# Kernel optimization log

Measured on AMD Instinct MI355X. Metric: run time of the kernel, lower is better.

Reference implementation:

```python
import jax, jax.numpy as jnp
import numpy as np

NHEAD = 16
DHEAD = 128  # dim_embed // nhead
ROPE_BASE = 10000.0


def rmsnorm(x, g):
    eps = jnp.finfo(x.dtype).eps  # torch nn.RMSNorm default eps=None -> dtype eps
    return x * jax.lax.rsqrt(jnp.mean(x * x, axis=-1, keepdims=True) + eps) * g


def rope(x):
    # torchtune-style interleaved RoPE. x: [B,S,H,D]
    B, S, H, D = x.shape
    freqs = 1.0 / (ROPE_BASE ** (jnp.arange(0, D, 2, dtype=jnp.float32) / D))  # [D/2]
    ang = jnp.arange(S, dtype=jnp.float32)[:, None] * freqs[None, :]           # [S,D/2]
    cos = jnp.cos(ang)[None, :, None, :]
    sin = jnp.sin(ang)[None, :, None, :]
    x1, x2 = x[..., 0::2], x[..., 1::2]
    return jnp.stack([x1 * cos - x2 * sin, x1 * sin + x2 * cos], axis=-1).reshape(B, S, H, D)


def setup_inputs() -> dict:
    key = jax.random.key(0)
    B, S, E, C = 4, 2048, 2048, 512
    ks = jax.random.split(key, 9)
    std = 0.02
    h = jax.random.normal(ks[0], (B, S, E), jnp.float32)
    w_d_kv = jax.random.normal(ks[1], (C, E), jnp.float32) * std
    w_u_k = jax.random.normal(ks[2], (E, C), jnp.float32) * std
    w_u_v = jax.random.normal(ks[3], (E, C), jnp.float32) * std
    w_d_q = jax.random.normal(ks[4], (C, E), jnp.float32) * std
    w_u_q = jax.random.normal(ks[5], (E, C), jnp.float32) * std
    w_kr = jax.random.normal(ks[6], (E, E), jnp.float32) * std
    w_qr = jax.random.normal(ks[7], (E, C), jnp.float32) * std
    w_o = jax.random.normal(ks[8], (E, E), jnp.float32) * std
    g1 = jnp.ones((C,), jnp.float32)
    g2 = jnp.ones((C,), jnp.float32)
    g3 = jnp.ones((E,), jnp.float32)
    return {"h": h, "w_d_kv": w_d_kv, "w_u_k": w_u_k, "w_u_v": w_u_v,
            "w_d_q": w_d_q, "w_u_q": w_u_q, "w_kr": w_kr, "w_qr": w_qr,
            "w_o": w_o, "g1": g1, "g2": g2, "g3": g3}


def reference(h, w_d_kv, w_u_k, w_u_v, w_d_q, w_u_q, w_kr, w_qr, w_o, g1, g2, g3):
    # Eval (inference) path of MLA with absorbed weights; no kv/kr cache.
    B, S, E = h.shape
    cq = rmsnorm(h @ w_d_q.T, g1)          # [B,S,C]
    ckv = rmsnorm(h @ w_d_kv.T, g2)        # [B,S,C]
    qr = rope((cq @ w_qr.T).reshape(B, S, NHEAD, DHEAD)).reshape(B, S, E)
    kr = rope((h @ w_kr.T).reshape(B, S, NHEAD, DHEAD)).reshape(B, S, E)
    # absorbed_w_q = (w_d_q.T @ w_u_q.T) @ w_u_k : [E,C]
    absorbed_w_q = (w_d_q.T @ w_u_q.T) @ w_u_k
    # absorbed_w_o = w_u_v.T @ w_o.T : [C,E]
    absorbed_w_o = w_u_v.T @ w_o.T
    aq = h @ absorbed_w_q                  # [B,S,C]  (note: raw h, as in source)
    scores = jnp.einsum('bsc,btc->bst', aq, ckv) + jnp.einsum('bse,bte->bst', qr, kr)
    attn = jax.nn.softmax(scores / np.float32(np.sqrt(NHEAD + DHEAD)), axis=-1)
    o = jnp.einsum('bst,btc->bsc', attn, ckv)
    u = rmsnorm(o @ absorbed_w_o, g3)      # [B,S,E]
    return (u, ckv, kr)
```

## Files before the change

kernel.cpp:

```cpp
#include <hip/hip_runtime.h>
#include <stdint.h>

typedef __attribute__((ext_vector_type(8))) short bf16x8;
typedef __attribute__((ext_vector_type(8))) unsigned short u16x8;
typedef __attribute__((ext_vector_type(4))) float floatx4;

__device__ __forceinline__ uint16_t f2bf(float f) {
  union { float f; uint32_t u; } v; v.f = f;
  uint32_t r = v.u + 0x7fffu + ((v.u >> 16) & 1u);
  return (uint16_t)(r >> 16);
}
__device__ __forceinline__ float bf2f(uint16_t b) {
  union { uint32_t u; float f; } v; v.u = ((uint32_t)b) << 16;
  return v.f;
}
__device__ __forceinline__ float ld_as_float(float v) { return v; }
__device__ __forceinline__ float ld_as_float(uint16_t v) { return bf2f(v); }

__device__ __forceinline__ void mfma16(floatx4& d, bf16x8 a, bf16x8 b) {
  asm("v_mfma_f32_16x16x32_bf16 %0, %1, %2, %0" : "+v"(d) : "v"(a), "v"(b));
}

#define FENCE() asm volatile("" ::: "memory")
#define SCHED() __builtin_amdgcn_sched_barrier(0)
#define SBAR()                                  \
  do {                                          \
    FENCE();                                    \
    __builtin_amdgcn_sched_barrier(0);          \
    __builtin_amdgcn_s_barrier();               \
    __builtin_amdgcn_sched_barrier(0);          \
    FENCE();                                    \
  } while (0)

template<int MODE>
__global__ void __launch_bounds__(512, 1) gemm256v3(
    const uint16_t* __restrict__ A, const uint16_t* __restrict__ B,
    void* __restrict__ C0v, void* __restrict__ C1v, void* __restrict__ C2v,
    int K, int lda, int ldb, int ldc,
    long sA, long sB, long sC, int swzG)
{
  __shared__ __attribute__((aligned(16))) char lds[131072];
  const int tid = threadIdx.x;
  const int w = tid >> 6, l = tid & 63;
  const int wm = w >> 2, wn = w & 3;

  const int gx = gridDim.x;
  const int nwg = gx * gridDim.y;
  int id = blockIdx.y * gx + blockIdx.x;
  if ((nwg & 7) == 0) id = (id & 7) * (nwg >> 3) + (id >> 3);
  const int grp = gx * swzG;
  const int ing = id % grp;
  const long bm = (long)(ing / swzG) * 256;
  const long bn = ((long)(id / grp) * swzG + (ing % swzG)) * 256;
  A += (long)blockIdx.z * sA;
  B += (long)blockIdx.z * sB;

  const int scol = (((l & 3) ^ ((l >> 3) & 3)) << 3);
  const uint16_t* gA = A + (bm + w * 16 + (l >> 2)) * (long)lda + scol;
  const uint16_t* gB = B + (bn + w * 16 + (l >> 2)) * (long)ldb + scol;
  const int ldsw = w * 1024;

#define STG_A3(slot, k0, r)                                                    \
  __builtin_amdgcn_global_load_lds(gA + (k0) + (long)(r) * 128 * lda,          \
      (uint16_t*)(lds + (slot) * 32768 + (r) * 8192 + ldsw), 16, 0, 0)
#define STG_B3(slot, k0, r)                                                    \
  __builtin_amdgcn_global_load_lds(gB + (k0) + (long)(r) * 128 * ldb,          \
      (uint16_t*)(lds + (slot) * 32768 + 16384 + (r) * 8192 + ldsw), 16, 0, 0)

  const int lr = l & 15;
  const int chunkx = (((l >> 4) ^ ((lr >> 1) & 3)) << 4);
  const int aoff = (wm * 128 + lr) * 64 + chunkx;
  const int boff = 16384 + (wn * 64 + lr) * 64 + chunkx;

  floatx4 acc[8][4];
#pragma unroll
  for (int i = 0; i < 8; i++)
#pragma unroll
    for (int j = 0; j < 4; j++) acc[i][j] = (floatx4){0.f, 0.f, 0.f, 0.f};

  const int nt = K >> 5;
#pragma unroll
  for (int tt = 0; tt < 3; tt++) {
    STG_A3(tt, tt * 32, 0); STG_A3(tt, tt * 32, 1);
    STG_B3(tt, tt * 32, 0); STG_B3(tt, tt * 32, 1);
  }
  asm volatile("s_waitcnt vmcnt(8)" ::: "memory");
  SBAR();

  bf16x8 Bf[4], Bfn[4], Af0[4], Af1[4];
#pragma unroll
  for (int j = 0; j < 4; j++) Bf[j] = *(const bf16x8*)(lds + boff + j * 1024);
#pragma unroll
  for (int i = 0; i < 4; i++) Af0[i] = *(const bf16x8*)(lds + aoff + i * 1024);

  for (int t = 0; t < nt; t++) {
    const char* Ls = lds + (t & 3) * 32768;
    const char* Ln = lds + ((t + 1) & 3) * 32768;
    const long pk0 = (long)(t + 3) << 5;
    const int pslot = (t + 3) & 3;
    const bool pf = (t + 3 < nt);

#pragma unroll
    for (int i = 0; i < 4; i++) Af1[i] = *(const bf16x8*)(Ls + aoff + (4 + i) * 1024);
    SCHED();
    if (pf) { STG_A3(pslot, pk0, 0); STG_A3(pslot, pk0, 1); }
    asm volatile("s_waitcnt lgkmcnt(4)" ::: "memory");
    SCHED();
    __builtin_amdgcn_s_setprio(1);
#pragma unroll
    for (int i = 0; i < 4; i++)
#pragma unroll
      for (int j = 0; j < 4; j++) mfma16(acc[i][j], Af0[i], Bf[j]);
    __builtin_amdgcn_s_setprio(0);
    SCHED();

    if (t + 3 < nt)      asm volatile("s_waitcnt vmcnt(6)" ::: "memory");
    else if (t + 2 < nt) asm volatile("s_waitcnt vmcnt(4)" ::: "memory");
    else if (t + 1 < nt) asm volatile("s_waitcnt vmcnt(0)" ::: "memory");
    asm volatile("s_waitcnt lgkmcnt(0)" ::: "memory");
    SBAR();

    if (t + 1 < nt) {
#pragma unroll
      for (int j = 0; j < 4; j++) Bfn[j] = *(const bf16x8*)(Ln + boff + j * 1024);
#pragma unroll
      for (int i = 0; i < 4; i++) Af0[i] = *(const bf16x8*)(Ln + aoff + i * 1024);
    }
    SCHED();
    if (pf) { STG_B3(pslot, pk0, 0); STG_B3(pslot, pk0, 1); }
    SCHED();
    __builtin_amdgcn_s_setprio(1);
#pragma unroll
    for (int i = 0; i < 4; i++)
#pragma unroll
      for (int j = 0; j < 4; j++) mfma16(acc[4 + i][j], Af1[i], Bf[j]);
    __builtin_amdgcn_s_setprio(0);
    SCHED();
#pragma unroll
    for (int j = 0; j < 4; j++) Bf[j] = Bfn[j];
  }
#undef STG_A3
#undef STG_B3

  const long crow = bm + wm * 128 + ((l >> 4) * 4);
  const long ccol = bn + wn * 64 + (l & 15);
  if constexpr (MODE == 0) {
    float* C = (float*)C0v + (long)blockIdx.z * sC;
#pragma unroll
    for (int i = 0; i < 8; i++)
#pragma unroll
      for (int r = 0; r < 4; r++) {
        long row = crow + i * 16 + r;
#pragma unroll
        for (int j = 0; j < 4; j++) C[row * (long)ldc + ccol + j * 16] = acc[i][j][r];
      }
  } else if constexpr (MODE == 1) {
    uint16_t* C = (uint16_t*)C0v + (long)blockIdx.z * sC;
#pragma unroll
    for (int i = 0; i < 8; i++)
#pragma unroll
      for (int r = 0; r < 4; r++) {
        long row = crow + i * 16 + r;
#pragma unroll
        for (int j = 0; j < 4; j++) C[row * (long)ldc + ccol + j * 16] = f2bf(acc[i][j][r]);
      }
  } else if constexpr (MODE == 3) {
    const float s = 1.0f / 12.0f;
    uint16_t* C = (uint16_t*)C0v + (long)blockIdx.z * sC;
#pragma unroll
    for (int i = 0; i < 8; i++)
#pragma unroll
      for (int r = 0; r < 4; r++) {
        long row = crow + i * 16 + r;
#pragma unroll
        for (int j = 0; j < 4; j++) C[row * (long)ldc + ccol + j * 16] = f2bf(acc[i][j][r] * s);
      }
  } else {
    if (bn < 512) {
      uint16_t* C = (uint16_t*)C0v;
#pragma unroll
      for (int i = 0; i < 8; i++)
#pragma unroll
        for (int r = 0; r < 4; r++) {
          long row = crow + i * 16 + r;
#pragma unroll
          for (int j = 0; j < 4; j++) C[row * 512 + ccol + j * 16] = f2bf(acc[i][j][r]);
        }
    } else if (bn < 1024) {
      float* C = (float*)C1v;
      const long cc = ccol - 512;
#pragma unroll
      for (int i = 0; i < 8; i++)
#pragma unroll
        for (int r = 0; r < 4; r++) {
          long row = crow + i * 16 + r;
#pragma unroll
          for (int j = 0; j < 4; j++) C[row * 512 + cc + j * 16] = acc[i][j][r];
        }
    } else {
      uint16_t* C = (uint16_t*)C2v;
      const long cc = ccol - 1024;
#pragma unroll
      for (int i = 0; i < 8; i++)
#pragma unroll
        for (int r = 0; r < 4; r++) {
          long row = crow + i * 16 + r;
#pragma unroll
          for (int j = 0; j < 4; j++) C[row * 2560 + cc + j * 16] = f2bf(acc[i][j][r]);
        }
    }
  }
}

template<int OUTB>
__global__ void __launch_bounds__(512, 2) gemm256(
    const uint16_t* __restrict__ A, const uint16_t* __restrict__ B,
    void* __restrict__ Cv, int K, int lda, int ldb, int ldc,
    long sA, long sB, long sC)
{
  __shared__ __attribute__((aligned(16))) char lds[147456];
  const int tid = threadIdx.x;
  const int w = tid >> 6, l = tid & 63;
  const int wm = w >> 1, wn = w & 1;

  const int gx = gridDim.x;
  const int nwg = gx * gridDim.y;
  int id = blockIdx.y * gx + blockIdx.x;
  if ((nwg & 7) == 0) id = (id & 7) * (nwg >> 3) + (id >> 3);
  const long bm = (long)(id % gx) * 256;
  const long bn = (long)(id / gx) * 128;
  A += (long)blockIdx.z * sA;
  B += (long)blockIdx.z * sB;

  const int sr = l >> 3;
  const int sc = l & 7;
  const int scol = ((sc ^ sr) << 3);
  const uint16_t* gA = A + (bm + w * 8 + sr) * (long)lda + scol;
  const uint16_t* gB = B + (bn + w * 8 + sr) * (long)ldb + scol;
  const int ldsw = w * 1024;

#define STAGE_A(bufi, k0, r)                                                     \
  __builtin_amdgcn_global_load_lds(gA + (k0) + (long)(r) * 64 * lda,             \
      (uint16_t*)(lds + (bufi) * 49152 + (r) * 8192 + ldsw), 16, 0, 0)
#define STAGE_B(bufi, k0, r)                                                     \
  __builtin_amdgcn_global_load_lds(gB + (k0) + (long)(r) * 64 * ldb,             \
      (uint16_t*)(lds + (bufi) * 49152 + 32768 + (r) * 8192 + ldsw), 16, 0, 0)

  const int lr = l & 15;
  const int kk = (l >> 4) << 4;
  const int msk = (l & 7) << 4;
  const int ko0 = kk ^ msk;
  const int ko1 = (64 + kk) ^ msk;
  const int arow = (wm * 64 + lr) * 128;
  const int brow = (wn * 64 + lr) * 128;

  floatx4 acc[4][4];
#pragma unroll
  for (int i = 0; i < 4; i++)
#pragma unroll
    for (int j = 0; j < 4; j++) acc[i][j] = (floatx4){0.f, 0.f, 0.f, 0.f};

  const int nt = K >> 6;
#pragma unroll
  for (int r = 0; r < 4; r++) STAGE_A(0, 0, r);
#pragma unroll
  for (int r = 0; r < 2; r++) STAGE_B(0, 0, r);
#pragma unroll
  for (int r = 0; r < 4; r++) STAGE_A(1, 64, r);
#pragma unroll
  for (int r = 0; r < 2; r++) STAGE_B(1, 64, r);
  asm volatile("s_waitcnt vmcnt(6)" ::: "memory");
  SBAR();

  bf16x8 af0[4], bf0[4], af1[4], bf1[4];
  {
    const char* LA = lds + arow;
    const char* LB = lds + 32768 + brow;
#pragma unroll
    for (int i = 0; i < 4; i++) af0[i] = *(const bf16x8*)(LA + i * 2048 + ko0);
#pragma unroll
    for (int j = 0; j < 4; j++) bf0[j] = *(const bf16x8*)(LB + j * 2048 + ko0);
  }

  for (int t = 0; t < nt; t++) {
    const int buf = t % 3;
    const int pbuf = (t + 2) % 3;
    const long pk0 = (long)(t + 2) << 6;
    const char* LA = lds + buf * 49152 + arow;
    const char* LB = lds + buf * 49152 + 32768 + brow;
    const bool pf = (t + 2 < nt);

    if (pf) { STAGE_A(pbuf, pk0, 0); STAGE_A(pbuf, pk0, 1); STAGE_B(pbuf, pk0, 0); }
#pragma unroll
    for (int i = 0; i < 4; i++) af1[i] = *(const bf16x8*)(LA + i * 2048 + ko1);
#pragma unroll
    for (int j = 0; j < 4; j++) bf1[j] = *(const bf16x8*)(LB + j * 2048 + ko1);
    SCHED();
    __builtin_amdgcn_s_setprio(1);
#pragma unroll
    for (int i = 0; i < 4; i++)
#pragma unroll
      for (int j = 0; j < 4; j++) mfma16(acc[i][j], af0[i], bf0[j]);
    __builtin_amdgcn_s_setprio(0);
    SCHED();

    if (pf) { STAGE_A(pbuf, pk0, 2); STAGE_A(pbuf, pk0, 3); STAGE_B(pbuf, pk0, 1); }
    if (t < nt - 2) asm volatile("s_waitcnt vmcnt(6) lgkmcnt(0)" ::: "memory");
    else            asm volatile("s_waitcnt vmcnt(0) lgkmcnt(0)" ::: "memory");
    SBAR();
    if (t < nt - 1) {
      const char* LAn = lds + ((t + 1) % 3) * 49152 + arow;
      const char* LBn = lds + ((t + 1) % 3) * 49152 + 32768 + brow;
#pragma unroll
      for (int i = 0; i < 4; i++) af0[i] = *(const bf16x8*)(LAn + i * 2048 + ko0);
#pragma unroll
      for (int j = 0; j < 4; j++) bf0[j] = *(const bf16x8*)(LBn + j * 2048 + ko0);
    }
    SCHED();
    __builtin_amdgcn_s_setprio(1);
#pragma unroll
    for (int i = 0; i < 4; i++)
#pragma unroll
      for (int j = 0; j < 4; j++) mfma16(acc[i][j], af1[i], bf1[j]);
    __builtin_amdgcn_s_setprio(0);
    SCHED();
  }
#undef STAGE_A
#undef STAGE_B

  const long crow = bm + wm * 64 + ((l >> 4) * 4);
  const long ccol = bn + wn * 64 + (l & 15);
  if constexpr (OUTB == 0) {
    float* C = (float*)Cv + (long)blockIdx.z * sC;
#pragma unroll
    for (int i = 0; i < 4; i++)
#pragma unroll
      for (int r = 0; r < 4; r++) {
        long row = crow + i * 16 + r;
#pragma unroll
        for (int j = 0; j < 4; j++) C[row * (long)ldc + ccol + j * 16] = acc[i][j][r];
      }
  } else {
    uint16_t* C = (uint16_t*)Cv + (long)blockIdx.z * sC;
#pragma unroll
    for (int i = 0; i < 4; i++)
#pragma unroll
      for (int r = 0; r < 4; r++) {
        long row = crow + i * 16 + r;
#pragma unroll
        for (int j = 0; j < 4; j++) C[row * (long)ldc + ccol + j * 16] = f2bf(acc[i][j][r]);
      }
  }
}

template<int OUTB>
__global__ void __launch_bounds__(256) gemm_bt(
    const uint16_t* __restrict__ A, const uint16_t* __restrict__ B,
    void* __restrict__ Cv, int K, int lda, int ldb, int ldc,
    long sA, long sB, long sC)
{
  __shared__ alignas(16) uint16_t As[4096];
  __shared__ alignas(16) uint16_t Bs[4096];
  const int tid = threadIdx.x;
  const int w = tid >> 6, l = tid & 63;
  const int wr = w >> 1, wc = w & 1;
  const long bm = (long)blockIdx.x * 128, bn = (long)blockIdx.y * 128;
  A += (long)blockIdx.z * sA;
  B += (long)blockIdx.z * sB;

  const uint16_t* ga0 = A + (bm + w * 16 + (l >> 2)) * (long)lda + (l & 3) * 8;
  const uint16_t* ga1 = ga0 + 64L * lda;
  const uint16_t* gb0 = B + (bn + w * 16 + (l >> 2)) * (long)ldb + (l & 3) * 8;
  const uint16_t* gb1 = gb0 + 64L * ldb;
  uint16_t* la0 = &As[w * 512];
  uint16_t* la1 = &As[2048 + w * 512];
  uint16_t* lb0 = &Bs[w * 512];
  uint16_t* lb1 = &Bs[2048 + w * 512];

  floatx4 acc[4][4];
#pragma unroll
  for (int i = 0; i < 4; i++)
#pragma unroll
    for (int j = 0; j < 4; j++) acc[i][j] = (floatx4){0.f, 0.f, 0.f, 0.f};

  const int rA = (wr * 64 + (l & 15)) * 32 + (l >> 4) * 8;
  const int rB = (wc * 64 + (l & 15)) * 32 + (l >> 4) * 8;

  for (int k0 = 0; k0 < K; k0 += 32) {
    __builtin_amdgcn_global_load_lds(ga0, la0, 16, 0, 0);
    __builtin_amdgcn_global_load_lds(ga1, la1, 16, 0, 0);
    __builtin_amdgcn_global_load_lds(gb0, lb0, 16, 0, 0);
    __builtin_amdgcn_global_load_lds(gb1, lb1, 16, 0, 0);
    ga0 += 32; ga1 += 32; gb0 += 32; gb1 += 32;
    __syncthreads();
    bf16x8 af[4], bfr[4];
#pragma unroll
    for (int i = 0; i < 4; i++) af[i] = *(const bf16x8*)&As[rA + i * 512];
#pragma unroll
    for (int j = 0; j < 4; j++) bfr[j] = *(const bf16x8*)&Bs[rB + j * 512];
#pragma unroll
    for (int i = 0; i < 4; i++)
#pragma unroll
      for (int j = 0; j < 4; j++) mfma16(acc[i][j], af[i], bfr[j]);
    __syncthreads();
  }

  const long crow = bm + wr * 64 + ((l >> 4) * 4);
  const long ccol = bn + wc * 64 + (l & 15);
  if constexpr (OUTB == 0) {
    float* C = (float*)Cv + (long)blockIdx.z * sC;
#pragma unroll
    for (int i = 0; i < 4; i++)
#pragma unroll
      for (int r = 0; r < 4; r++) {
        long row = crow + i * 16 + r;
#pragma unroll
        for (int j = 0; j < 4; j++) C[row * (long)ldc + ccol + j * 16] = acc[i][j][r];
      }
  } else {
    uint16_t* C = (uint16_t*)Cv + (long)blockIdx.z * sC;
#pragma unroll
    for (int i = 0; i < 4; i++)
#pragma unroll
      for (int r = 0; r < 4; r++) {
        long row = crow + i * 16 + r;
#pragma unroll
        for (int j = 0; j < 4; j++) C[row * (long)ldc + ccol + j * 16] = f2bf(acc[i][j][r]);
      }
  }
}

__global__ void __launch_bounds__(256) reduceK(const float* __restrict__ in,
                                               uint16_t* __restrict__ out,
                                               long n, int S, long stride) {
  long i = ((long)blockIdx.x * 256 + threadIdx.x) * 4;
  if (i >= n) return;
  float4 s = *(const float4*)(in + i);
  for (int k = 1; k < S; k++) {
    float4 t = *(const float4*)(in + k * stride + i);
    s.x += t.x; s.y += t.y; s.z += t.z; s.w += t.w;
  }
  ushort4 o; o.x = f2bf(s.x); o.y = f2bf(s.y); o.z = f2bf(s.z); o.w = f2bf(s.w);
  *(ushort4*)(out + i) = o;
}

__global__ void __launch_bounds__(256) prep_all(
    const float* __restrict__ h,
    const float* __restrict__ wdq, const float* __restrict__ wdkv,
    const float* __restrict__ wqr, const float* __restrict__ wkr,
    const float* __restrict__ wo,
    uint16_t* __restrict__ hb,
    uint16_t* __restrict__ wdq_b, uint16_t* __restrict__ wdkv_b,
    uint16_t* __restrict__ wqr_b, uint16_t* __restrict__ wkr_b,
    uint16_t* __restrict__ wo_b, float2* __restrict__ rtab)
{
  const int b = blockIdx.x;
  if (b < 27648) {
    const float* src; uint16_t* dst; long off;
    if (b < 16384)      { src = h;    dst = hb;     off = b; }
    else if (b < 17408) { src = wdq;  dst = wdq_b;  off = b - 16384; }
    else if (b < 18432) { src = wdkv; dst = wdkv_b; off = b - 17408; }
    else if (b < 19456) { src = wqr;  dst = wqr_b;  off = b - 18432; }
    else if (b < 23552) { src = wkr;  dst = wkr_b;  off = b - 19456; }
    else                { src = wo;   dst = wo_b;   off = b - 23552; }
    long i = (off * 256 + threadIdx.x) * 4;
    float4 v = *(const float4*)(src + i);
    ushort4 o; o.x = f2bf(v.x); o.y = f2bf(v.y); o.z = f2bf(v.z); o.w = f2bf(v.w);
    *(ushort4*)(dst + i) = o;
  } else {
    int idx = (b - 27648) * 256 + threadIdx.x;
    int s = idx >> 6, fi = idx & 63;
    float f = powf(10000.0f, -(float)fi * (1.0f / 64.0f));
    float ang = (float)s * f;
    rtab[idx] = make_float2(cosf(ang), sinf(ang));
  }
}

template<typename TIN>
__global__ void __launch_bounds__(256) transpose_to_bf16(
    const TIN* __restrict__ in, uint16_t* __restrict__ out,
    int ld_in, int ld_out, long sIn, long sOut)
{
  __shared__ float tile[32][33];
  in += (long)blockIdx.z * sIn;
  out += (long)blockIdx.z * sOut;
  const int rb = blockIdx.y * 32, cb = blockIdx.x * 32;
#pragma unroll
  for (int i = 0; i < 32; i += 8)
    tile[threadIdx.y + i][threadIdx.x] =
        ld_as_float(in[(long)(rb + threadIdx.y + i) * ld_in + cb + threadIdx.x]);
  __syncthreads();
#pragma unroll
  for (int i = 0; i < 32; i += 8)
    out[(long)(cb + threadIdx.y + i) * ld_out + rb + threadIdx.x] =
        f2bf(tile[threadIdx.x][threadIdx.y + i]);
}

template<int PT, typename TIN>
__global__ void __launch_bounds__(256) rmsnorm_k(
    const TIN* __restrict__ in, const float* __restrict__ g,
    float* __restrict__ out_f, uint16_t* __restrict__ out_b, int ld_b)
{
  constexpr int DIM = PT * 256;
  __shared__ float sm[9];
  const TIN* x = in + (long)blockIdx.x * DIM;
  const int base = threadIdx.x * PT;
  float v[PT];
  if constexpr (sizeof(TIN) == 2) {
    if constexpr (PT >= 8) {
#pragma unroll
      for (int i = 0; i < PT; i += 8) {
        u16x8 t = *(const u16x8*)&x[base + i];
#pragma unroll
        for (int q = 0; q < 8; q++) v[i + q] = bf2f(t[q]);
      }
    } else {
#pragma unroll
      for (int i = 0; i < PT; i += 2) {
        ushort2 t = *(const ushort2*)&x[base + i];
        v[i] = bf2f(t.x); v[i + 1] = bf2f(t.y);
      }
    }
  } else if constexpr (PT == 2) {
    float2 t = *(const float2*)&x[base]; v[0] = t.x; v[1] = t.y;
  } else {
#pragma unroll
    for (int i = 0; i < PT; i += 4) {
      float4 t = *(const float4*)&x[base + i];
      v[i] = t.x; v[i + 1] = t.y; v[i + 2] = t.z; v[i + 3] = t.w;
    }
  }
  float ss = 0.f;
#pragma unroll
  for (int i = 0; i < PT; i++) ss += v[i] * v[i];
#pragma unroll
  for (int o = 32; o; o >>= 1) ss += __shfl_down(ss, o);
  if ((threadIdx.x & 63) == 0) sm[threadIdx.x >> 6] = ss;
  __syncthreads();
  if (threadIdx.x == 0)
    sm[8] = rsqrtf((sm[0] + sm[1] + sm[2] + sm[3]) * (1.0f / DIM) + 1.1920929e-7f);
  __syncthreads();
  const float sc = sm[8];
#pragma unroll
  for (int i = 0; i < PT; i++) {
    float y = v[i] * sc * g[base + i];
    if (out_f) out_f[(long)blockIdx.x * DIM + base + i] = y;
    if (out_b) out_b[(long)blockIdx.x * ld_b + base + i] = f2bf(y);
  }
}

template<bool WF32>
__global__ void __launch_bounds__(256) rope_k(
    const uint16_t* __restrict__ in, uint16_t* __restrict__ outb,
    float* __restrict__ outf, const float2* __restrict__ tab)
{
  long idx = (long)blockIdx.x * 256 + threadIdx.x;
  int r = (int)(idx >> 10);
  int pp = (int)idx & 1023;
  int s = r & 2047;
  int fi = pp & 63;
  ushort2 xv = *(const ushort2*)(in + ((long)r << 11) + 2 * pp);
  float x0 = bf2f(xv.x), x1 = bf2f(xv.y);
  float2 cs = tab[(s << 6) + fi];
  float y0 = x0 * cs.x - x1 * cs.y;
  float y1 = x0 * cs.y + x1 * cs.x;
  ushort2 ov; ov.x = f2bf(y0); ov.y = f2bf(y1);
  *(ushort2*)(outb + (long)r * 2560 + 512 + 2 * pp) = ov;
  if (WF32) *(float2*)(outf + ((long)r << 11) + 2 * pp) = make_float2(y0, y1);
}

__global__ void __launch_bounds__(256) softmax_k(const uint16_t* __restrict__ sc,
                                                 uint16_t* __restrict__ attn) {
  __shared__ float sm[9];
  const uint16_t* x = sc + ((long)blockIdx.x << 11);
  const int base = threadIdx.x * 8;
  float v[8];
  u16x8 t = *(const u16x8*)&x[base];
#pragma unroll
  for (int i = 0; i < 8; i++) v[i] = bf2f(t[i]);
  float m = -1e30f;
#pragma unroll
  for (int i = 0; i < 8; i++) m = fmaxf(m, v[i]);
#pragma unroll
  for (int o = 32; o; o >>= 1) m = fmaxf(m, __shfl_down(m, o));
  if ((threadIdx.x & 63) == 0) sm[threadIdx.x >> 6] = m;
  __syncthreads();
  if (threadIdx.x == 0)
    sm[8] = fmaxf(fmaxf(sm[0], sm[1]), fmaxf(sm[2], sm[3]));
  __syncthreads();
  m = sm[8];
  __syncthreads();
  float ss = 0.f;
#pragma unroll
  for (int i = 0; i < 8; i++) { v[i] = __expf(v[i] - m); ss += v[i]; }
#pragma unroll
  for (int o = 32; o; o >>= 1) ss += __shfl_down(ss, o);
  if ((threadIdx.x & 63) == 0) sm[threadIdx.x >> 6] = ss;
  __syncthreads();
  if (threadIdx.x == 0) sm[8] = 1.0f / (sm[0] + sm[1] + sm[2] + sm[3]);
  __syncthreads();
  const float r = sm[8];
  ushort4 o1, o2;
  o1.x = f2bf(v[0] * r); o1.y = f2bf(v[1] * r); o1.z = f2bf(v[2] * r); o1.w = f2bf(v[3] * r);
  o2.x = f2bf(v[4] * r); o2.y = f2bf(v[5] * r); o2.z = f2bf(v[6] * r); o2.w = f2bf(v[7] * r);
  uint16_t* dst = attn + ((long)blockIdx.x << 11) + base;
  *(ushort4*)dst = o1;
  *(ushort4*)(dst + 4) = o2;
}

extern "C" void kernel_launch(void* const* d_in, const int* in_sizes, int n_in,
                              void* d_out, int out_size, void* d_ws, size_t ws_size,
                              hipStream_t stream) {
  (void)in_sizes; (void)n_in; (void)out_size; (void)ws_size;
  const float* h    = (const float*)d_in[0];
  const float* wdkv = (const float*)d_in[1];
  const float* wuk  = (const float*)d_in[2];
  const float* wuv  = (const float*)d_in[3];
  const float* wdq  = (const float*)d_in[4];
  const float* wuq  = (const float*)d_in[5];
  const float* wkr  = (const float*)d_in[6];
  const float* wqr  = (const float*)d_in[7];
  const float* wo   = (const float*)d_in[8];
  const float* g1   = (const float*)d_in[9];
  const float* g2   = (const float*)d_in[10];
  const float* g3   = (const float*)d_in[11];

  float* u_out   = (float*)d_out;
  float* ckv_out = u_out + 16777216L;
  float* kr_out  = ckv_out + 4194304L;

  char* p = (char*)d_ws;
  auto alloc = [&](size_t bytes) -> void* {
    void* q = (void*)p; p += (bytes + 255) & ~(size_t)255; return q;
  };
  uint16_t* hb     = (uint16_t*)alloc(16777216ULL * 2);
  uint16_t* wcat   = (uint16_t*)alloc(3145728ULL * 2);
  uint16_t* wqr_b  = (uint16_t*)alloc(1048576ULL * 2);
  uint16_t* wkr_b  = (uint16_t*)alloc(4194304ULL * 2);
  uint16_t* wo_b   = (uint16_t*)alloc(4194304ULL * 2);
  uint16_t* wukT   = (uint16_t*)alloc(1048576ULL * 2);
  uint16_t* wuqT   = (uint16_t*)alloc(1048576ULL * 2);
  uint16_t* wuvT   = (uint16_t*)alloc(1048576ULL * 2);
  uint16_t* wdqT   = (uint16_t*)alloc(1048576ULL * 2);
  uint16_t* T1t    = (uint16_t*)alloc(262144ULL * 2);
  uint16_t* awoT   = (uint16_t*)alloc(1048576ULL * 2);
  uint16_t* cqpre  = (uint16_t*)alloc(4194304ULL * 2);
  uint16_t* cq_b   = (uint16_t*)alloc(4194304ULL * 2);
  uint16_t* catq   = (uint16_t*)alloc(20971520ULL * 2);
  uint16_t* catk   = (uint16_t*)alloc(20971520ULL * 2);
  uint16_t* ckvT   = (uint16_t*)alloc(4194304ULL * 2);
  uint16_t* o_b    = (uint16_t*)alloc(4194304ULL * 2);
  float2*   rtab   = (float2*)alloc(131072ULL * 8);
  float*    tmpS2  = (float*)alloc(4194304ULL * 4);
  float*    tmpB   = (float*)alloc(16777216ULL * 4);
  float*    redT   = (float*)alloc(1048576ULL * 4);
  float*    redW   = (float*)alloc(4194304ULL * 4);
  uint16_t* tmpBb  = (uint16_t*)tmpB;
  uint16_t* attn   = catq;

  uint16_t* wdq_b  = wcat;
  uint16_t* wdkv_b = wcat + 1048576;
  uint16_t* Bqt    = wcat + 2097152;

  const dim3 b256(256);
  const dim3 b512(512);
  const dim3 tb(32, 8);

  prep_all<<<dim3(28160), b256, 0, stream>>>(
      h, wdq, wdkv, wqr, wkr, wo, hb, wdq_b, wdkv_b, wqr_b, wkr_b, wo_b, rtab);
  transpose_to_bf16<float><<<dim3(16, 64, 1), tb, 0, stream>>>(wuk, wukT, 512, 2048, 0, 0);
  transpose_to_bf16<float><<<dim3(16, 64, 1), tb, 0, stream>>>(wuq, wuqT, 512, 2048, 0, 0);
  transpose_to_bf16<float><<<dim3(16, 64, 1), tb, 0, stream>>>(wuv, wuvT, 512, 2048, 0, 0);
  transpose_to_bf16<float><<<dim3(64, 16, 1), tb, 0, stream>>>(wdq, wdqT, 2048, 512, 0, 0);

  gemm_bt<0><<<dim3(4, 4, 4), b256, 0, stream>>>(
      wukT, wuqT, redT, 512, 2048, 2048, 512, 512L, 512L, 262144L);
  reduceK<<<dim3(256), b256, 0, stream>>>(redT, T1t, 262144L, 4, 262144L);
  gemm_bt<0><<<dim3(16, 4, 4), b256, 0, stream>>>(
      wo_b, wuvT, redW, 512, 2048, 2048, 512, 512L, 512L, 1048576L);
  reduceK<<<dim3(1024), b256, 0, stream>>>(redW, awoT, 1048576L, 4, 1048576L);
  gemm_bt<1><<<dim3(4, 16, 1), b256, 0, stream>>>(T1t, wdqT, Bqt, 512, 512, 512, 2048, 0, 0, 0);

  gemm256v3<2><<<dim3(32, 6, 1), b512, 0, stream>>>(
      hb, wcat, cqpre, tmpS2, catq, 2048, 2048, 2048, 0, 0, 0, 0, 2);
  rmsnorm_k<2, uint16_t><<<dim3(8192), b256, 0, stream>>>(cqpre, g1, nullptr, cq_b, 512);
  gemm256v3<1><<<dim3(32, 8, 1), b512, 0, stream>>>(
      cq_b, wqr_b, tmpBb, nullptr, nullptr, 512, 512, 512, 2048, 0, 0, 0, 4);
  rope_k<false><<<dim3(32768), b256, 0, stream>>>(tmpBb, catq, nullptr, rtab);
  rmsnorm_k<2, float><<<dim3(8192), b256, 0, stream>>>(tmpS2, g2, ckv_out, catk, 2560);
  transpose_to_bf16<uint16_t><<<dim3(16, 64, 4), tb, 0, stream>>>(
      catk, ckvT, 2560, 2048, 2048L * 2560, 512L * 2048);
  gemm256v3<1><<<dim3(32, 8, 1), b512, 0, stream>>>(
      hb, wkr_b, tmpBb, nullptr, nullptr, 2048, 2048, 2048, 2048, 0, 0, 0, 4);
  rope_k<true><<<dim3(32768), b256, 0, stream>>>(tmpBb, catk, kr_out, rtab);
  gemm256v3<3><<<dim3(8, 8, 4), b512, 0, stream>>>(
      catq, catk, tmpBb, nullptr, nullptr, 2560, 2560, 2560, 2048,
      5242880L, 5242880L, 4194304L, 2);
  softmax_k<<<dim3(8192), b256, 0, stream>>>(tmpBb, attn);
  gemm256<1><<<dim3(8, 4, 4), b512, 0, stream>>>(
      attn, ckvT, o_b, 2048, 2048, 2048, 512, 4194304L, 1048576L, 1048576L);
  gemm256v3<1><<<dim3(32, 8, 1), b512, 0, stream>>>(
      o_b, awoT, tmpBb, nullptr, nullptr, 512, 512, 512, 2048, 0, 0, 0, 4);
  rmsnorm_k<8, uint16_t><<<dim3(8192), b256, 0, stream>>>(tmpBb, g3, u_out, nullptr, 0);
}
```

Baseline: 493.9 us.

## Fuse RoPE into GEMM epilogues and merge four weight transposes into one launch

The qr and kr projection GEMMs now apply interleaved RoPE in their epilogue, getting each pair partner through a lane shuffle and writing straight into the concatenated q/k buffers (plus the fp32 kr output). This removes two standalone rope kernels and the bf16 round trip through a temporary buffer. The four separate weight transpose launches are also merged into a single kernel. The fused path depends on adjacent output columns sitting in adjacent lanes of the MFMA accumulator layout, and it does extra table loads and scattered scalar stores in the epilogue.

```diff
diff --git a/kernel.cpp b/kernel.cpp
--- a/kernel.cpp
+++ b/kernel.cpp
@@ -174,6 +174,28 @@
         long row = crow + i * 16 + r;
 #pragma unroll
         for (int j = 0; j < 4; j++) C[row * (long)ldc + ccol + j * 16] = f2bf(acc[i][j][r] * s);
+      }
+  } else if constexpr (MODE == 4 || MODE == 5) {
+    const float2* __restrict__ tab = (const float2*)C1v;
+    uint16_t* Cb = (uint16_t*)C0v;
+    float* Cf = (float*)C2v;
+    const float sgn = (l & 1) ? 1.0f : -1.0f;
+#pragma unroll
+    for (int i = 0; i < 8; i++)
+#pragma unroll
+      for (int r = 0; r < 4; r++) {
+        long row = crow + i * 16 + r;
+        const float2* trow = tab + (((int)(row & 2047)) << 6);
+#pragma unroll
+        for (int j = 0; j < 4; j++) {
+          long c = ccol + j * 16;
+          float v = acc[i][j][r];
+          float pp = __shfl_xor(v, 1);
+          float2 cs = trow[((int)(c & 127)) >> 1];
+          float y = v * cs.x + sgn * pp * cs.y;
+          Cb[row * 2560 + 512 + c] = f2bf(y);
+          if constexpr (MODE == 5) Cf[row * 2048 + c] = y;
+        }
       }
   } else {
     if (bn < 512) {
@@ -476,6 +498,37 @@
   }
 }
 
+__global__ void __launch_bounds__(256) transpose4(
+    const float* __restrict__ wuk, const float* __restrict__ wuq,
+    const float* __restrict__ wuv, const float* __restrict__ wdq,
+    uint16_t* __restrict__ wukT, uint16_t* __restrict__ wuqT,
+    uint16_t* __restrict__ wuvT, uint16_t* __restrict__ wdqT)
+{
+  __shared__ float tile[32][33];
+  const int bt = blockIdx.x;
+  const float* in; uint16_t* out; int ld_in, ld_out, rb, cb;
+  if (bt < 3072) {
+    const int op = bt >> 10, rem = bt & 1023;
+    in = (op == 0) ? wuk : (op == 1) ? wuq : wuv;
+    out = (op == 0) ? wukT : (op == 1) ? wuqT : wuvT;
+    ld_in = 512; ld_out = 2048;
+    cb = (rem & 15) * 32; rb = (rem >> 4) * 32;
+  } else {
+    const int rem = bt - 3072;
+    in = wdq; out = wdqT; ld_in = 2048; ld_out = 512;
+    cb = (rem & 63) * 32; rb = (rem >> 6) * 32;
+  }
+#pragma unroll
+  for (int i = 0; i < 32; i += 8)
+    tile[threadIdx.y + i][threadIdx.x] =
+        in[(long)(rb + threadIdx.y + i) * ld_in + cb + threadIdx.x];
+  __syncthreads();
+#pragma unroll
+  for (int i = 0; i < 32; i += 8)
+    out[(long)(cb + threadIdx.y + i) * ld_out + rb + threadIdx.x] =
+        f2bf(tile[threadIdx.x][threadIdx.y + i]);
+}
+
 template<typename TIN>
 __global__ void __launch_bounds__(256) transpose_to_bf16(
     const TIN* __restrict__ in, uint16_t* __restrict__ out,
@@ -547,26 +600,6 @@
     if (out_f) out_f[(long)blockIdx.x * DIM + base + i] = y;
     if (out_b) out_b[(long)blockIdx.x * ld_b + base + i] = f2bf(y);
   }
-}
-
-template<bool WF32>
-__global__ void __launch_bounds__(256) rope_k(
-    const uint16_t* __restrict__ in, uint16_t* __restrict__ outb,
-    float* __restrict__ outf, const float2* __restrict__ tab)
-{
-  long idx = (long)blockIdx.x * 256 + threadIdx.x;
-  int r = (int)(idx >> 10);
-  int pp = (int)idx & 1023;
-  int s = r & 2047;
-  int fi = pp & 63;
-  ushort2 xv = *(const ushort2*)(in + ((long)r << 11) + 2 * pp);
-  float x0 = bf2f(xv.x), x1 = bf2f(xv.y);
-  float2 cs = tab[(s << 6) + fi];
-  float y0 = x0 * cs.x - x1 * cs.y;
-  float y1 = x0 * cs.y + x1 * cs.x;
-  ushort2 ov; ov.x = f2bf(y0); ov.y = f2bf(y1);
-  *(ushort2*)(outb + (long)r * 2560 + 512 + 2 * pp) = ov;
-  if (WF32) *(float2*)(outf + ((long)r << 11) + 2 * pp) = make_float2(y0, y1);
 }
 
 __global__ void __launch_bounds__(256) softmax_k(const uint16_t* __restrict__ sc,
@@ -668,10 +701,8 @@
 
   prep_all<<<dim3(28160), b256, 0, stream>>>(
       h, wdq, wdkv, wqr, wkr, wo, hb, wdq_b, wdkv_b, wqr_b, wkr_b, wo_b, rtab);
-  transpose_to_bf16<float><<<dim3(16, 64, 1), tb, 0, stream>>>(wuk, wukT, 512, 2048, 0, 0);
-  transpose_to_bf16<float><<<dim3(16, 64, 1), tb, 0, stream>>>(wuq, wuqT, 512, 2048, 0, 0);
-  transpose_to_bf16<float><<<dim3(16, 64, 1), tb, 0, stream>>>(wuv, wuvT, 512, 2048, 0, 0);
-  transpose_to_bf16<float><<<dim3(64, 16, 1), tb, 0, stream>>>(wdq, wdqT, 2048, 512, 0, 0);
+  transpose4<<<dim3(4096), tb, 0, stream>>>(
+      wuk, wuq, wuv, wdq, wukT, wuqT, wuvT, wdqT);
 
   gemm_bt<0><<<dim3(4, 4, 4), b256, 0, stream>>>(
       wukT, wuqT, redT, 512, 2048, 2048, 512, 512L, 512L, 262144L);
@@ -684,15 +715,13 @@
   gemm256v3<2><<<dim3(32, 6, 1), b512, 0, stream>>>(
       hb, wcat, cqpre, tmpS2, catq, 2048, 2048, 2048, 0, 0, 0, 0, 2);
   rmsnorm_k<2, uint16_t><<<dim3(8192), b256, 0, stream>>>(cqpre, g1, nullptr, cq_b, 512);
-  gemm256v3<1><<<dim3(32, 8, 1), b512, 0, stream>>>(
-      cq_b, wqr_b, tmpBb, nullptr, nullptr, 512, 512, 512, 2048, 0, 0, 0, 4);
-  rope_k<false><<<dim3(32768), b256, 0, stream>>>(tmpBb, catq, nullptr, rtab);
+  gemm256v3<4><<<dim3(32, 8, 1), b512, 0, stream>>>(
+      cq_b, wqr_b, catq, rtab, nullptr, 512, 512, 512, 2560, 0, 0, 0, 4);
   rmsnorm_k<2, float><<<dim3(8192), b256, 0, stream>>>(tmpS2, g2, ckv_out, catk, 2560);
   transpose_to_bf16<uint16_t><<<dim3(16, 64, 4), tb, 0, stream>>>(
       catk, ckvT, 2560, 2048, 2048L * 2560, 512L * 2048);
-  gemm256v3<1><<<dim3(32, 8, 1), b512, 0, stream>>>(
-      hb, wkr_b, tmpBb, nullptr, nullptr, 2048, 2048, 2048, 2048, 0, 0, 0, 4);
-  rope_k<true><<<dim3(32768), b256, 0, stream>>>(tmpBb, catk, kr_out, rtab);
+  gemm256v3<5><<<dim3(32, 8, 1), b512, 0, stream>>>(
+      hb, wkr_b, catk, rtab, kr_out, 2048, 2048, 2048, 2560, 0, 0, 0, 4);
   gemm256v3<3><<<dim3(8, 8, 4), b512, 0, stream>>>(
       catq, catk, tmpBb, nullptr, nullptr, 2560, 2560, 2560, 2048,
       5242880L, 5242880L, 4194304L, 2);
```

After: 472.2 us. 1.05x faster.
